# Kernel optimization log

Measured on AMD Instinct MI355X. Metric: run time of the kernel, lower is better.

The kernel has to match this reference:

```python
import jax, jax.numpy as jnp
import numpy as np

B, T, I, H = 64, 1024, 256, 512


def setup_inputs() -> dict:
    key = jax.random.key(0)
    ks = jax.random.split(key, 5)
    # Xavier-uniform-like scale: sqrt(6/(fan_in+fan_out)) ~ use small normal init
    def xavier(k, shape):
        bound = np.sqrt(6.0 / (shape[0] + shape[1])).astype(np.float32)
        return jax.random.uniform(k, shape, jnp.float32, -bound, bound)
    return {
        "x": jax.random.normal(ks[0], (B, T, I), jnp.float32),
        "W_ih0": xavier(ks[1], (I, H)),
        "W_hh0": xavier(ks[2], (H, H)),
        "b0": jnp.zeros((H,), jnp.float32),
        "W_ih1": xavier(ks[3], (H, H)),
        "W_hh1": xavier(ks[4], (H, H)),
        "b1": jnp.zeros((H,), jnp.float32),
    }


def _run_layer(xs, W_ih, W_hh, b):
    # xs: [B, T, D_in] -> ys: [B, T, H], h_last: [B, H]
    h0 = jnp.zeros((xs.shape[0], W_hh.shape[0]), xs.dtype)
    # Precompute input transform for all timesteps in one big GEMM
    x_proj = jnp.einsum('btd,dh->bth', xs, W_ih)

    def step(h, xp_t):
        h_new = jnp.tanh(xp_t + h @ W_hh + b)
        return h_new, h_new

    h_last, ys = jax.lax.scan(step, h0, jnp.swapaxes(x_proj, 0, 1))  # scan over T
    return jnp.swapaxes(ys, 0, 1), h_last


def reference(x, W_ih0, W_hh0, b0, W_ih1, W_hh1, b1):
    out0, h0n = _run_layer(x, W_ih0, W_hh0, b0)
    out1, h1n = _run_layer(out0, W_ih1, W_hh1, b1)
    h_n = jnp.stack([h0n, h1n], axis=0)  # [num_layers, B, H]
    return out1, h_n
```

## Files before the change

kernel.cpp:

```cpp
#include <hip/hip_runtime.h>
#include <cstdint>

#define B_  64
#define T_  1024
#define I_  256
#define H_  512

typedef _Float16 h2_t __attribute__((ext_vector_type(2)));
typedef int sv16 __attribute__((ext_vector_type(16)));

__device__ __forceinline__ uint16_t f2h(float f) {
  _Float16 h = (_Float16)f;
  return __builtin_bit_cast(uint16_t, h);
}
__device__ __forceinline__ float dot2(uint32_t a, uint32_t b, float c) {
  return __builtin_amdgcn_fdot2(__builtin_bit_cast(h2_t, a),
                                __builtin_bit_cast(h2_t, b), c, false);
}
__device__ __forceinline__ float fast_tanh(float s) {
  float e = __expf(2.0f * s);
  return fmaf(-2.0f, __builtin_amdgcn_rcpf(e + 1.0f), 1.0f);
}

template<int P>
__device__ __forceinline__ uint32_t hsel(sv16 h0, sv16 h1, sv16 h2, sv16 h3) {
  if constexpr (P < 16)      return (uint32_t)h0[P];
  else if constexpr (P < 32) return (uint32_t)h1[P - 16];
  else if constexpr (P < 48) return (uint32_t)h2[P - 32];
  else                       return (uint32_t)h3[P - 48];
}

__global__ void pack_whh(const float* __restrict__ W, uint32_t* __restrict__ out) {
  int idx = blockIdx.x * 256 + threadIdx.x;
  int k8 = idx >> 11;
  int j  = (idx >> 2) & 511;
  int m  = idx & 3;
  int k  = k8 * 8 + m * 2;
  uint32_t lo = f2h(W[k * H_ + j]);
  uint32_t hi = f2h(W[(k + 1) * H_ + j]);
  out[idx] = lo | (hi << 16);
}

template<int K>
__global__ __launch_bounds__(256) void gemm_rows(const float* A,
    const float* __restrict__ W, const float* __restrict__ bias,
    float* Y) {
  __shared__ float As[64 * (K + 1)];
  const int tid = threadIdx.x;
  const size_t row0 = (size_t)blockIdx.x * 64;
  const float* Ab = A + row0 * K;
  for (int idx = tid * 4; idx < 64 * K; idx += 1024) {
    float4 v = *(const float4*)(Ab + idx);
    int rr = idx / K;
    int cc = idx - rr * K;
    float* dst = &As[rr * (K + 1) + cc];
    dst[0] = v.x; dst[1] = v.y; dst[2] = v.z; dst[3] = v.w;
  }
  __syncthreads();
  const int cg = tid & 15;
  const int rg = tid >> 4;
  float acc[4][32];
  #pragma unroll
  for (int i = 0; i < 32; ++i) {
    float bz = bias[cg + 16 * i];
    acc[0][i] = bz; acc[1][i] = bz; acc[2][i] = bz; acc[3][i] = bz;
  }
  const float* Wc = W + cg;
  for (int k = 0; k < K; ++k) {
    float a0 = As[(rg * 4 + 0) * (K + 1) + k];
    float a1 = As[(rg * 4 + 1) * (K + 1) + k];
    float a2 = As[(rg * 4 + 2) * (K + 1) + k];
    float a3 = As[(rg * 4 + 3) * (K + 1) + k];
    const float* Wk = Wc + (size_t)k * H_;
    #pragma unroll
    for (int i = 0; i < 32; ++i) {
      float w = Wk[16 * i];
      acc[0][i] = fmaf(a0, w, acc[0][i]);
      acc[1][i] = fmaf(a1, w, acc[1][i]);
      acc[2][i] = fmaf(a2, w, acc[2][i]);
      acc[3][i] = fmaf(a3, w, acc[3][i]);
    }
  }
  float* Yb = Y + row0 * H_;
  #pragma unroll
  for (int jj = 0; jj < 4; ++jj) {
    float* Yr = Yb + (size_t)(rg * 4 + jj) * H_ + cg;
    #pragma unroll
    for (int i = 0; i < 32; ++i) Yr[16 * i] = acc[jj][i];
  }
}

#define ROW(m, WEXPR) { uint4 w_ = (WEXPR); \
  a0 = dot2(w_.x, hsel<4*(m)+0>(h0,h1,h2,h3), a0); \
  a1 = dot2(w_.y, hsel<4*(m)+1>(h0,h1,h2,h3), a1); \
  a2 = dot2(w_.z, hsel<4*(m)+2>(h0,h1,h2,h3), a2); \
  a3 = dot2(w_.w, hsel<4*(m)+3>(h0,h1,h2,h3), a3); }

#define BATCH_LOAD(OFF0, OFF1, OFF2, OFF3) \
  asm volatile("s_load_dwordx16 %0, %4, " OFF0 "\n\t" \
               "s_load_dwordx16 %1, %4, " OFF1 "\n\t" \
               "s_load_dwordx16 %2, %4, " OFF2 "\n\t" \
               "s_load_dwordx16 %3, %4, " OFF3 "\n\t" \
               "s_waitcnt lgkmcnt(0)" \
               : "=&s"(h0), "=&s"(h1), "=&s"(h2), "=&s"(h3) : "s"(hbase)); \
  __builtin_amdgcn_sched_barrier(0);

#define CONS16(W0)  ROW(0,W0(0))  ROW(1,W0(1))  ROW(2,W0(2))  ROW(3,W0(3)) \
                    ROW(4,W0(4))  ROW(5,W0(5))  ROW(6,W0(6))  ROW(7,W0(7)) \
                    ROW(8,W0(8))  ROW(9,W0(9))  ROW(10,W0(10)) ROW(11,W0(11)) \
                    ROW(12,W0(12)) ROW(13,W0(13)) ROW(14,W0(14)) ROW(15,W0(15))

#define WREG0(m) wrv[m]
#define WREG1(m) wrv[16 + (m)]
#define WLDS(m)  WL[(m) * 512 + j]
#define WSTR(m)  g[m]

__global__ __launch_bounds__(512, 2) void rnn_scan(float* Y,
    const uint4* __restrict__ Wp, ushort* __restrict__ hb16,
    float* __restrict__ hn) {
  __shared__ uint4 WL[16 * 512];
  const int j = threadIdx.x;
  float* Yb = Y + (size_t)blockIdx.x * (T_ * H_);
  ushort* hp0 = hb16 + blockIdx.x * (2 * H_);
  ushort* hp1 = hp0 + H_;

  uint4 wrv[32];
  #pragma unroll
  for (int m = 0; m < 32; ++m) wrv[m] = Wp[m * H_ + j];
  #pragma unroll
  for (int it = 0; it < 16; ++it) WL[it * 512 + j] = Wp[(32 + it) * 512 + j];

  float xp0 = Yb[j];
  float v = fast_tanh(xp0);
  hp0[j] = f2h(v);
  Yb[j] = v;
  const uint64_t hb0 = (uint64_t)(uintptr_t)hp0;
  const uint64_t hb1 = (uint64_t)(uintptr_t)hp1;
  asm volatile("s_waitcnt vmcnt(0) lgkmcnt(0)\n\ts_barrier\n\ts_dcache_inv" ::: "memory");

  for (int t = 1; t < T_; ++t) {
    const uint64_t hbase = (t & 1) ? hb0 : hb1;
    ushort* hst = (t & 1) ? hp1 : hp0;
    float xpt = Yb[t * H_ + j];
    uint4 g[16];
    #pragma unroll
    for (int m = 0; m < 16; ++m) g[m] = Wp[(48 + m) * H_ + j];
    float a0 = 0.f, a1 = 0.f, a2 = 0.f, a3 = 0.f;
    sv16 h0, h1, h2, h3;

    BATCH_LOAD("0x0", "0x40", "0x80", "0xc0")
    CONS16(WREG0)
    BATCH_LOAD("0x100", "0x140", "0x180", "0x1c0")
    CONS16(WREG1)
    BATCH_LOAD("0x200", "0x240", "0x280", "0x2c0")
    CONS16(WLDS)
    BATCH_LOAD("0x300", "0x340", "0x380", "0x3c0")
    CONS16(WSTR)

    float s = xpt + ((a0 + a1) + (a2 + a3));
    v = fast_tanh(s);
    hst[j] = f2h(v);
    asm volatile("s_waitcnt vmcnt(0)\n\ts_barrier\n\ts_dcache_inv" ::: "memory");
    Yb[t * H_ + j] = v;
  }
  hn[blockIdx.x * H_ + j] = v;
}

extern "C" void kernel_launch(void* const* d_in, const int* in_sizes, int n_in,
                              void* d_out, int out_size, void* d_ws, size_t ws_size,
                              hipStream_t stream) {
  const float* x     = (const float*)d_in[0];
  const float* W_ih0 = (const float*)d_in[1];
  const float* W_hh0 = (const float*)d_in[2];
  const float* b0    = (const float*)d_in[3];
  const float* W_ih1 = (const float*)d_in[4];
  const float* W_hh1 = (const float*)d_in[5];
  const float* b1    = (const float*)d_in[6];

  float* Y  = (float*)d_out;
  float* hn = Y + (size_t)B_ * T_ * H_;
  uint32_t* Wp = (uint32_t*)d_ws;
  ushort* hbuf = (ushort*)((char*)d_ws + 512 * 1024);

  pack_whh<<<512, 256, 0, stream>>>(W_hh0, Wp);
  gemm_rows<I_><<<1024, 256, 0, stream>>>(x, W_ih0, b0, Y);
  rnn_scan<<<B_, H_, 0, stream>>>(Y, (const uint4*)Wp, hbuf, hn);
  pack_whh<<<512, 256, 0, stream>>>(W_hh1, Wp);
  gemm_rows<H_><<<1024, 256, 0, stream>>>(Y, W_ih1, b1, Y);
  rnn_scan<<<B_, H_, 0, stream>>>(Y, (const uint4*)Wp, hbuf, hn + B_ * H_);
}
```

Before: 4.103 ms.

## Replace FP32 input-projection GEMM with FP16 MFMA kernel using prepacked weights

The scalar-FMA input projection GEMM is replaced with a kernel using 16x16x32 f16 MFMA instructions. A new pack kernel converts W_ih into fp16 fragments laid out per lane, and the activation tile is converted to fp16 in XOR-swizzled shared memory. This targets the cost of the two large per-layer projection GEMMs, which run outside the sequential scan. The trade-off is reduced precision on the projection inputs and an extra packing launch per layer.

```diff
diff --git a/kernel.cpp b/kernel.cpp
--- a/kernel.cpp
+++ b/kernel.cpp
@@ -8,10 +8,12 @@
 
 typedef _Float16 h2_t __attribute__((ext_vector_type(2)));
 typedef int sv16 __attribute__((ext_vector_type(16)));
-
-__device__ __forceinline__ uint16_t f2h(float f) {
+typedef _Float16 f16x8 __attribute__((ext_vector_type(8)));
+typedef float f32x4 __attribute__((ext_vector_type(4)));
+
+__device__ __forceinline__ uint32_t f2h(float f) {
   _Float16 h = (_Float16)f;
-  return __builtin_bit_cast(uint16_t, h);
+  return (uint32_t)__builtin_bit_cast(uint16_t, h);
 }
 __device__ __forceinline__ float dot2(uint32_t a, uint32_t b, float c) {
   return __builtin_amdgcn_fdot2(__builtin_bit_cast(h2_t, a),
@@ -42,51 +44,81 @@
 }
 
 template<int K>
-__global__ __launch_bounds__(256) void gemm_rows(const float* A,
-    const float* __restrict__ W, const float* __restrict__ bias,
-    float* Y) {
-  __shared__ float As[64 * (K + 1)];
+__global__ __launch_bounds__(512) void pack_wih(const float* __restrict__ W,
+                                                uint4* __restrict__ out) {
+  constexpr int KS = K / 32;
+  int t = blockIdx.x * 512 + threadIdx.x;
+  int l  = t & 63;
+  int ks = (t >> 6) % KS;
+  int cb = t / (64 * KS);
+  int c  = cb * 16 + (l & 15);
+  int k0 = ks * 32 + ((l >> 4) & 3) * 8;
+  uint4 u;
+  u.x = f2h(W[(k0 + 0) * H_ + c]) | (f2h(W[(k0 + 1) * H_ + c]) << 16);
+  u.y = f2h(W[(k0 + 2) * H_ + c]) | (f2h(W[(k0 + 3) * H_ + c]) << 16);
+  u.z = f2h(W[(k0 + 4) * H_ + c]) | (f2h(W[(k0 + 5) * H_ + c]) << 16);
+  u.w = f2h(W[(k0 + 6) * H_ + c]) | (f2h(W[(k0 + 7) * H_ + c]) << 16);
+  out[t] = u;
+}
+
+template<int K>
+__global__ __launch_bounds__(512) void gemm_mfma(const float* A,
+    const uint4* __restrict__ WT, const float* __restrict__ bias, float* Y) {
+  constexpr int KS = K / 32;
+  __shared__ __align__(16) char As[64 * K * 2];
   const int tid = threadIdx.x;
   const size_t row0 = (size_t)blockIdx.x * 64;
-  const float* Ab = A + row0 * K;
-  for (int idx = tid * 4; idx < 64 * K; idx += 1024) {
-    float4 v = *(const float4*)(Ab + idx);
-    int rr = idx / K;
-    int cc = idx - rr * K;
-    float* dst = &As[rr * (K + 1) + cc];
-    dst[0] = v.x; dst[1] = v.y; dst[2] = v.z; dst[3] = v.w;
+
+  const float4* Ab4 = (const float4*)(A + row0 * K);
+  #pragma unroll
+  for (int it = 0; it < K / 32; ++it) {
+    int i4 = tid + it * 512;
+    int fi = i4 * 4;
+    int row = fi / K;
+    int kk  = fi - row * K;
+    float4 v = Ab4[i4];
+    uint2 u;
+    u.x = f2h(v.x) | (f2h(v.y) << 16);
+    u.y = f2h(v.z) | (f2h(v.w) << 16);
+    int off = row * (2 * K) + ((kk * 2) ^ ((row & 7) << 4));
+    *(uint2*)(As + off) = u;
   }
   __syncthreads();
-  const int cg = tid & 15;
-  const int rg = tid >> 4;
-  float acc[4][32];
-  #pragma unroll
-  for (int i = 0; i < 32; ++i) {
-    float bz = bias[cg + 16 * i];
-    acc[0][i] = bz; acc[1][i] = bz; acc[2][i] = bz; acc[3][i] = bz;
-  }
-  const float* Wc = W + cg;
-  for (int k = 0; k < K; ++k) {
-    float a0 = As[(rg * 4 + 0) * (K + 1) + k];
-    float a1 = As[(rg * 4 + 1) * (K + 1) + k];
-    float a2 = As[(rg * 4 + 2) * (K + 1) + k];
-    float a3 = As[(rg * 4 + 3) * (K + 1) + k];
-    const float* Wk = Wc + (size_t)k * H_;
+
+  const int lane = tid & 63;
+  const int wv   = tid >> 6;
+  const int rw   = wv >> 1;
+  const int ch   = wv & 1;
+
+  f32x4 acc[16];
+  #pragma unroll
+  for (int cf = 0; cf < 16; ++cf) {
+    float bz = bias[ch * 256 + cf * 16 + (lane & 15)];
+    acc[cf] = (f32x4){bz, bz, bz, bz};
+  }
+
+  const int arow = rw * 16 + (lane & 15);
+  const int abase = arow * (2 * K);
+  const int aswz = (arow & 7) << 4;
+  for (int ks = 0; ks < KS; ++ks) {
+    int kbyte = ks * 64 + ((lane >> 4) & 3) * 16;
+    f16x8 af = *(const f16x8*)(As + abase + (kbyte ^ aswz));
     #pragma unroll
-    for (int i = 0; i < 32; ++i) {
-      float w = Wk[16 * i];
-      acc[0][i] = fmaf(a0, w, acc[0][i]);
-      acc[1][i] = fmaf(a1, w, acc[1][i]);
-      acc[2][i] = fmaf(a2, w, acc[2][i]);
-      acc[3][i] = fmaf(a3, w, acc[3][i]);
+    for (int cf = 0; cf < 16; ++cf) {
+      uint4 bu = WT[(size_t)((ch * 16 + cf) * KS + ks) * 64 + lane];
+      f16x8 bf = __builtin_bit_cast(f16x8, bu);
+      acc[cf] = __builtin_amdgcn_mfma_f32_16x16x32_f16(af, bf, acc[cf], 0, 0, 0);
     }
   }
-  float* Yb = Y + row0 * H_;
-  #pragma unroll
-  for (int jj = 0; jj < 4; ++jj) {
-    float* Yr = Yb + (size_t)(rg * 4 + jj) * H_ + cg;
+  __syncthreads();
+
+  const int wrow = rw * 16 + ((lane >> 4) & 3) * 4;
+  #pragma unroll
+  for (int cf = 0; cf < 16; ++cf) {
+    int col = ch * 256 + cf * 16 + (lane & 15);
+    float* Yp = Y + (row0 + wrow) * H_ + col;
     #pragma unroll
-    for (int i = 0; i < 32; ++i) Yr[16 * i] = acc[jj][i];
+    for (int r = 0; r < 4; ++r) Yp[r * H_] = acc[cf][r];
   }
 }
 
@@ -132,7 +164,7 @@
 
   float xp0 = Yb[j];
   float v = fast_tanh(xp0);
-  hp0[j] = f2h(v);
+  hp0[j] = (ushort)f2h(v);
   Yb[j] = v;
   const uint64_t hb0 = (uint64_t)(uintptr_t)hp0;
   const uint64_t hb1 = (uint64_t)(uintptr_t)hp1;
@@ -159,7 +191,7 @@
 
     float s = xpt + ((a0 + a1) + (a2 + a3));
     v = fast_tanh(s);
-    hst[j] = f2h(v);
+    hst[j] = (ushort)f2h(v);
     asm volatile("s_waitcnt vmcnt(0)\n\ts_barrier\n\ts_dcache_inv" ::: "memory");
     Yb[t * H_ + j] = v;
   }
@@ -181,11 +213,14 @@
   float* hn = Y + (size_t)B_ * T_ * H_;
   uint32_t* Wp = (uint32_t*)d_ws;
   ushort* hbuf = (ushort*)((char*)d_ws + 512 * 1024);
+  uint4* WT  = (uint4*)((char*)d_ws + 640 * 1024);
 
   pack_whh<<<512, 256, 0, stream>>>(W_hh0, Wp);
-  gemm_rows<I_><<<1024, 256, 0, stream>>>(x, W_ih0, b0, Y);
+  pack_wih<I_><<<32, 512, 0, stream>>>(W_ih0, WT);
+  gemm_mfma<I_><<<1024, 512, 0, stream>>>(x, WT, b0, Y);
   rnn_scan<<<B_, H_, 0, stream>>>(Y, (const uint4*)Wp, hbuf, hn);
   pack_whh<<<512, 256, 0, stream>>>(W_hh1, Wp);
-  gemm_rows<H_><<<1024, 256, 0, stream>>>(Y, W_ih1, b1, Y);
+  pack_wih<H_><<<64, 512, 0, stream>>>(W_ih1, WT);
+  gemm_mfma<H_><<<1024, 512, 0, stream>>>(Y, WT, b1, Y);
   rnn_scan<<<B_, H_, 0, stream>>>(Y, (const uint4*)Wp, hbuf, hn + B_ * H_);
 }
```

New measurement: 3.352 ms. -18.3%, faster.
